# Kernel tuning notes

Hardware: AMD Instinct MI355X
Metric: run time of the kernel (lower is better)

Reference implementation:

```python
import jax, jax.numpy as jnp
import numpy as np

B, S, D_IN = 16, 1024, 1024
H, D_OUT = 16, 128

def setup_inputs() -> dict:
    key = jax.random.key(0)
    k1, k2, k3 = jax.random.split(key, 3)
    x = jax.random.normal(k1, (B, S, D_IN), dtype=jnp.float32)
    W = jax.random.normal(k2, (H, 3, D_IN, D_OUT), dtype=jnp.float32) * (1.0 / np.sqrt(D_IN))
    Wo = jax.random.normal(k3, (H * D_OUT, D_OUT), dtype=jnp.float32) * (1.0 / np.sqrt(H * D_OUT))
    return {"x": x, "W": W, "Wo": Wo}

def reference(x, W, Wo):
    # x: [B,S,D_IN], W: [H,3,D_IN,E], Wo: [H*E,E]
    E = W.shape[-1]
    q = jnp.einsum('bsd,hde->bhse', x, W[:, 0])
    k = jnp.einsum('bsd,hde->bhse', x, W[:, 1])
    v = jnp.einsum('bsd,hde->bhse', x, W[:, 2])
    # NOTE: source divides by (output_dim * 0.5), not sqrt(output_dim)
    scores = jnp.einsum('bhse,bhte->bhst', q, k) / (E * 0.5)
    attn = jax.nn.softmax(scores, axis=-1)
    o = jnp.einsum('bhst,bhte->bhse', attn, v)          # [B,H,S,E]
    o = jnp.transpose(o, (0, 2, 1, 3)).reshape(x.shape[0], x.shape[1], -1)  # concat heads
    return jnp.einsum('bsf,fe->bse', o, Wo)
```

## Files before the change

kernel.cpp:

```cpp
#include <hip/hip_runtime.h>

typedef unsigned short u16;
typedef _Float16 f16;
typedef __attribute__((ext_vector_type(8))) _Float16 half8;
typedef __attribute__((ext_vector_type(8))) short short8;
typedef __attribute__((ext_vector_type(4))) float f32x4;
typedef __attribute__((ext_vector_type(4))) float f4;
typedef __attribute__((ext_vector_type(4))) u16 u16x4;

#define B_ 16
#define S_ 1024
#define DIN_ 1024
#define H_ 16
#define E_ 128

#define EXPK 0.0225546041776533f

__device__ __forceinline__ u16 f2h(float f) {
  f16 h = (f16)f;
  return __builtin_bit_cast(u16, h);
}

__device__ __forceinline__ void gl2lds16(const u16* g, u16* l) {
  __builtin_amdgcn_global_load_lds((const __attribute__((address_space(1))) void*)g,
                                   (__attribute__((address_space(3))) void*)l, 16, 0, 0);
}

__global__ __launch_bounds__(256) void zero_f32(float* __restrict__ p) {
  int i = (blockIdx.x * 256 + threadIdx.x) * 4;
  f4 z = {0.f, 0.f, 0.f, 0.f};
  *reinterpret_cast<f4*>(p + i) = z;
}

__global__ __launch_bounds__(256) void cvt_f32_f16(const float* __restrict__ in,
                                                   u16* __restrict__ out) {
  int i = (blockIdx.x * 256 + threadIdx.x) * 4;
  f4 v = *reinterpret_cast<const f4*>(in + i);
  u16x4 o;
  o[0] = f2h(v[0]); o[1] = f2h(v[1]); o[2] = f2h(v[2]); o[3] = f2h(v[3]);
  *reinterpret_cast<u16x4*>(out + i) = o;
}

__global__ __launch_bounds__(256) void transpose_cvt(const float* __restrict__ in,
                                                     u16* __restrict__ out,
                                                     int R, int C) {
  __shared__ float tile[32][33];
  const size_t moff = (size_t)blockIdx.z * R * C;
  const float* src = in + moff;
  u16* dst = out + moff;
  int c0 = blockIdx.x * 32, r0 = blockIdx.y * 32;
  int tx = threadIdx.x & 31, ty = threadIdx.x >> 5;
#pragma unroll
  for (int i = 0; i < 32; i += 8)
    tile[ty + i][tx] = src[(size_t)(r0 + ty + i) * C + c0 + tx];
  __syncthreads();
#pragma unroll
  for (int i = 0; i < 32; i += 8)
    dst[(size_t)(c0 + ty + i) * R + r0 + tx] = f2h(tile[tx][ty + i]);
}

template<int MODE, int KSPLIT, int K>
__global__ __launch_bounds__(256) void gemm_bt(const u16* __restrict__ A,
                                               const u16* __restrict__ BT,
                                               u16* __restrict__ q, u16* __restrict__ kk,
                                               u16* __restrict__ vT, float* __restrict__ out) {
  const int tid = threadIdx.x;
  const int m0 = blockIdx.x * 128;
  const u16* Bblk = BT + (size_t)blockIdx.y * 128 * K;
  __shared__ __align__(16) u16 smem[132 * 128];
  u16* As = smem;
  u16* Bs = smem + 8192;
  const int w = tid >> 6, lane = tid & 63;
  const int quad = lane >> 4, ln = lane & 15;
  const int wr = w >> 1, wc = w & 1;

  const int kbeg = (KSPLIT > 1) ? blockIdx.z * (K / KSPLIT) : 0;
  constexpr int KLEN = K / KSPLIT;

  const int rr = lane >> 3;
  const int cc = (lane & 7) ^ rr;
  const u16* agp[4];
  const u16* bgp[4];
#pragma unroll
  for (int i = 0; i < 4; i++) {
    int row = i * 32 + w * 8 + rr;
    agp[i] = A + (size_t)(m0 + row) * K + kbeg + cc * 8;
    bgp[i] = Bblk + (size_t)row * K + kbeg + cc * 8;
  }

  int offA[4][2], offB[4][2];
#pragma unroll
  for (int mt = 0; mt < 4; mt++) {
    int row = wr * 64 + mt * 16 + ln;
#pragma unroll
    for (int k2 = 0; k2 < 2; k2++)
      offA[mt][k2] = row * 64 + (((k2 * 4 + quad) ^ (ln & 7)) * 8);
  }
#pragma unroll
  for (int nt = 0; nt < 4; nt++) {
    int row = wc * 64 + nt * 16 + ln;
#pragma unroll
    for (int k2 = 0; k2 < 2; k2++)
      offB[nt][k2] = row * 64 + (((k2 * 4 + quad) ^ (ln & 7)) * 8);
  }

  f32x4 acc[4][4];
  f32x4 zero = {0.f, 0.f, 0.f, 0.f};
#pragma unroll
  for (int mt = 0; mt < 4; mt++)
#pragma unroll
    for (int nt = 0; nt < 4; nt++) acc[mt][nt] = zero;

#pragma unroll
  for (int k0 = 0; k0 < KLEN; k0 += 64) {
    __syncthreads();
#pragma unroll
    for (int i = 0; i < 4; i++) {
      gl2lds16(agp[i] + k0, As + i * 2048 + w * 512);
      gl2lds16(bgp[i] + k0, Bs + i * 2048 + w * 512);
    }
    __syncthreads();
#pragma unroll
    for (int k2 = 0; k2 < 2; k2++) {
      half8 af[4], bfr[4];
#pragma unroll
      for (int mt = 0; mt < 4; mt++)
        af[mt] = *reinterpret_cast<const half8*>(&As[offA[mt][k2]]);
#pragma unroll
      for (int nt = 0; nt < 4; nt++)
        bfr[nt] = *reinterpret_cast<const half8*>(&Bs[offB[nt][k2]]);
#pragma unroll
      for (int mt = 0; mt < 4; mt++)
#pragma unroll
        for (int nt = 0; nt < 4; nt++)
          acc[mt][nt] = __builtin_amdgcn_mfma_f32_16x16x32_f16(af[mt], bfr[nt], acc[mt][nt], 0, 0, 0);
    }
  }

  if (MODE == 0) {
    const int h = blockIdx.y / 3, c = blockIdx.y % 3;
    if (c < 2) {
      u16* dst = (c == 0) ? q : kk;
      const float sc = (c == 0) ? EXPK : 1.0f;
#pragma unroll
      for (int mt = 0; mt < 4; mt++)
#pragma unroll
        for (int nt = 0; nt < 4; nt++)
#pragma unroll
          for (int r = 0; r < 4; r++) {
            int row = wr * 64 + mt * 16 + quad * 4 + r;
            int tok = m0 + row;
            int bb = tok >> 10, s = tok & 1023;
            int e = wc * 64 + nt * 16 + ln;
            dst[(((size_t)bb * H_ + h) * S_ + s) * E_ + e] = f2h(acc[mt][nt][r] * sc);
          }
    } else {
      __syncthreads();
#pragma unroll
      for (int mt = 0; mt < 4; mt++)
#pragma unroll
        for (int nt = 0; nt < 4; nt++)
#pragma unroll
          for (int r = 0; r < 4; r++) {
            int row = wr * 64 + mt * 16 + quad * 4 + r;
            int e = wc * 64 + nt * 16 + ln;
            smem[e * 132 + row] = f2h(acc[mt][nt][r]);
          }
      __syncthreads();
      const int bb = m0 >> 10, sbase = m0 & 1023;
      u16* vbase = vT + (((size_t)bb * H_ + h) * E_) * S_;
#pragma unroll
      for (int i = 0; i < 8; i++) {
        int e = (tid >> 4) + i * 16, s0 = (tid & 15) * 8;
        *reinterpret_cast<short8*>(&vbase[(size_t)e * S_ + sbase + s0]) =
            *reinterpret_cast<const short8*>(&smem[e * 132 + s0]);
      }
    }
  } else {
#pragma unroll
    for (int mt = 0; mt < 4; mt++)
#pragma unroll
      for (int nt = 0; nt < 4; nt++)
#pragma unroll
        for (int r = 0; r < 4; r++) {
          int row = wr * 64 + mt * 16 + quad * 4 + r;
          int e = wc * 64 + nt * 16 + ln;
          if (KSPLIT > 1)
            atomicAdd(&out[(size_t)(m0 + row) * E_ + e], acc[mt][nt][r]);
          else
            out[(size_t)(m0 + row) * E_ + e] = acc[mt][nt][r];
        }
  }
}

struct SmemKVP {
  u16 ks[64 * 128];
  u16 vs[128 * 64];
  u16 ps[128 * 68];
};
union SmemAttn {
  u16 qs[128 * 132];
  SmemKVP s;
};

__global__ __launch_bounds__(256, 3) void attn_kernel(const u16* __restrict__ qg,
                                                      const u16* __restrict__ kg,
                                                      const u16* __restrict__ vg,
                                                      u16* __restrict__ og) {
  __shared__ __align__(16) SmemAttn sm;
  const int tid = threadIdx.x;
  const int id = blockIdx.x;
  const int g = id >> 6, qt = (id >> 3) & 7, x = id & 7;
  const int hb = g * 8 + x;
  const int b = hb >> 4, h = hb & 15;
  const int q0 = qt * 128;
  const size_t bh = (size_t)(b * H_ + h);
  const u16* qp = qg + bh * S_ * E_;
  const u16* kp = kg + bh * S_ * E_;
  const u16* vp = vg + bh * E_ * S_;
  const int w = tid >> 6, lane = tid & 63, quad = lane >> 4, ln = lane & 15;

#pragma unroll
  for (int i = 0; i < 8; i++) {
    int idx = tid + i * 256;
    int row = idx >> 4, col = (idx & 15) * 8;
    *reinterpret_cast<short8*>(&sm.qs[row * 132 + col]) =
        *reinterpret_cast<const short8*>(&qp[(size_t)(q0 + row) * E_ + col]);
  }
  __syncthreads();
  half8 qf[2][4];
#pragma unroll
  for (int mt = 0; mt < 2; mt++)
#pragma unroll
    for (int ks = 0; ks < 4; ks++)
      qf[mt][ks] = *reinterpret_cast<const half8*>(
          &sm.qs[(w * 32 + mt * 16 + ln) * 132 + ks * 32 + quad * 8]);

  const int krow = w * 4 + (lane >> 4);
  const int kc = ((lane & 15) & 8) | (((lane & 15) & 7) ^ (krow & 7));
  const u16* kbase = kp + (size_t)krow * E_ + kc * 8;
  const int vrow = w * 8 + (lane >> 3);
  const int vc = (lane & 7) ^ ((lane >> 3) & 7);
  const u16* vbase = vp + (size_t)vrow * S_ + vc * 8;

  f32x4 zero = {0.f, 0.f, 0.f, 0.f};
  f32x4 oa[2][8];
#pragma unroll
  for (int mt = 0; mt < 2; mt++)
#pragma unroll
    for (int nt = 0; nt < 8; nt++) oa[mt][nt] = zero;
  float lsum[2][4];
#pragma unroll
  for (int mt = 0; mt < 2; mt++)
#pragma unroll
    for (int r = 0; r < 4; r++) lsum[mt][r] = 0.f;

  for (int kt = 0; kt < 16; kt++) {
    __syncthreads();
#pragma unroll
    for (int i = 0; i < 4; i++) {
      gl2lds16(kbase + (size_t)kt * 8192 + i * 16 * E_, &sm.s.ks[(i * 256 + w * 64) * 8]);
      gl2lds16(vbase + (size_t)kt * 64 + i * 32 * S_,   &sm.s.vs[(i * 256 + w * 64) * 8]);
    }
    __syncthreads();

    f32x4 sa[2][4];
#pragma unroll
    for (int mt = 0; mt < 2; mt++)
#pragma unroll
      for (int nt = 0; nt < 4; nt++) sa[mt][nt] = zero;
#pragma unroll
    for (int ks = 0; ks < 4; ks++) {
      half8 kf[4];
#pragma unroll
      for (int nt = 0; nt < 4; nt++) {
        int c = ks * 4 + quad;
        int cs = (c & 8) | ((c & 7) ^ (ln & 7));
        kf[nt] = *reinterpret_cast<const half8*>(&sm.s.ks[(nt * 16 + ln) * 128 + cs * 8]);
      }
#pragma unroll
      for (int mt = 0; mt < 2; mt++)
#pragma unroll
        for (int nt = 0; nt < 4; nt++)
          sa[mt][nt] = __builtin_amdgcn_mfma_f32_16x16x32_f16(qf[mt][ks], kf[nt], sa[mt][nt], 0, 0, 0);
    }

#pragma unroll
    for (int mt = 0; mt < 2; mt++) {
#pragma unroll
      for (int r = 0; r < 4; r++) {
        int prow = (w * 32 + mt * 16 + quad * 4 + r) * 68;
        float psum = 0.f;
#pragma unroll
        for (int nt = 0; nt < 4; nt++) {
          float p = exp2f(sa[mt][nt][r]);
          psum += p;
          sm.s.ps[prow + nt * 16 + ln] = f2h(p);
        }
        lsum[mt][r] += psum;
      }
    }

#pragma unroll
    for (int k2 = 0; k2 < 2; k2++) {
      half8 pf[2];
#pragma unroll
      for (int mt = 0; mt < 2; mt++)
        pf[mt] = *reinterpret_cast<const half8*>(
            &sm.s.ps[(w * 32 + mt * 16 + ln) * 68 + k2 * 32 + quad * 8]);
#pragma unroll
      for (int nt8 = 0; nt8 < 8; nt8++) {
        int c = k2 * 4 + quad;
        int cs = c ^ (ln & 7);
        half8 vf = *reinterpret_cast<const half8*>(&sm.s.vs[(nt8 * 16 + ln) * 64 + cs * 8]);
#pragma unroll
        for (int mt = 0; mt < 2; mt++)
          oa[mt][nt8] = __builtin_amdgcn_mfma_f32_16x16x32_f16(pf[mt], vf, oa[mt][nt8], 0, 0, 0);
      }
    }
  }

#pragma unroll
  for (int mt = 0; mt < 2; mt++) {
#pragma unroll
    for (int r = 0; r < 4; r++) {
      float l = lsum[mt][r];
#pragma unroll
      for (int d = 1; d < 16; d <<= 1) l += __shfl_xor(l, d);
      float rl = 1.0f / l;
      int srow = q0 + w * 32 + mt * 16 + quad * 4 + r;
      size_t base = ((size_t)b * S_ + srow) * (H_ * E_) + (size_t)h * E_;
#pragma unroll
      for (int nt8 = 0; nt8 < 8; nt8++)
        og[base + nt8 * 16 + ln] = f2h(oa[mt][nt8][r] * rl);
    }
  }
}

extern "C" void kernel_launch(void* const* d_in, const int* in_sizes, int n_in,
                              void* d_out, int out_size, void* d_ws, size_t ws_size,
                              hipStream_t stream) {
  const float* x = (const float*)d_in[0];
  const float* W = (const float*)d_in[1];
  const float* Wo = (const float*)d_in[2];
  float* out = (float*)d_out;
  char* ws = (char*)d_ws;

  const size_t WBT_BYTES = (size_t)H_ * 3 * DIN_ * E_ * 2;
  const size_t WOT_BYTES = (size_t)H_ * E_ * E_ * 2 * 2;
  const size_t FIXED = WBT_BYTES + WOT_BYTES;

  const size_t XB_PER   = (size_t)S_ * DIN_ * 2;
  const size_t QKV_PER  = (size_t)H_ * S_ * E_ * 2;
  const size_t OB_PER   = (size_t)S_ * H_ * E_ * 2;
  const size_t PER_ITEM = XB_PER + 3 * QKV_PER + OB_PER;

  int Bc = 1;
  for (int c = 16; c >= 1; c >>= 1) {
    if (FIXED + (size_t)c * PER_ITEM <= ws_size) { Bc = c; break; }
  }

  u16* WbT = (u16*)(ws);
  u16* WoT = (u16*)(ws + WBT_BYTES);
  char* cb = ws + FIXED;
  u16* xb  = (u16*)(cb);
  u16* qb  = (u16*)(cb + (size_t)Bc * XB_PER);
  u16* kb  = (u16*)(cb + (size_t)Bc * (XB_PER + QKV_PER));
  u16* vTb = (u16*)(cb + (size_t)Bc * (XB_PER + 2 * QKV_PER));
  u16* ob  = (u16*)(cb + (size_t)Bc * (XB_PER + 3 * QKV_PER));

  zero_f32<<<out_size / 1024, 256, 0, stream>>>(out);
  transpose_cvt<<<dim3(4, 32, 48), 256, 0, stream>>>(W, WbT, DIN_, E_);
  transpose_cvt<<<dim3(4, 64, 1), 256, 0, stream>>>(Wo, WoT, H_ * E_, E_);

  for (int b0 = 0; b0 < B_; b0 += Bc) {
    const float* xc = x + (size_t)b0 * S_ * DIN_;
    cvt_f32_f16<<<Bc * S_ * DIN_ / 1024, 256, 0, stream>>>(xc, xb);
    gemm_bt<0, 1, DIN_><<<dim3(Bc * 8, 48), 256, 0, stream>>>(xb, WbT, qb, kb, vTb, nullptr);
    attn_kernel<<<Bc * 128, 256, 0, stream>>>(qb, kb, vTb, ob);
    gemm_bt<1, 4, H_ * E_><<<dim3(Bc * 8, 1, 4), 256, 0, stream>>>(ob, WoT, nullptr, nullptr,
                                                                   nullptr, out + (size_t)b0 * S_ * E_);
  }
}
```

Baseline: 565.0 us.

## Keep softmax probabilities in registers by computing transposed S=K·Qᵀ

The QK^T MFMA now has its operands swapped so each lane holds score values for one query and four consecutive keys. The exp2 results are packed to fp16 in registers and used directly as the A operand of the PV MFMA, which removes the LDS round trip for P and the ps buffer. V fragments are now read as two half4 loads to match the new key ordering. Row sums are reduced across quads and redistributed with a shuffle at the end. The trade-off is more, smaller LDS reads for V in exchange for less shared memory, with possible occupancy gains.

```diff
diff --git a/kernel.cpp b/kernel.cpp
--- a/kernel.cpp
+++ b/kernel.cpp
@@ -3,6 +3,8 @@
 typedef unsigned short u16;
 typedef _Float16 f16;
 typedef __attribute__((ext_vector_type(8))) _Float16 half8;
+typedef __attribute__((ext_vector_type(4))) _Float16 half4;
+typedef __attribute__((ext_vector_type(2))) _Float16 half2v;
 typedef __attribute__((ext_vector_type(8))) short short8;
 typedef __attribute__((ext_vector_type(4))) float f32x4;
 typedef __attribute__((ext_vector_type(4))) float f4;
@@ -19,6 +21,10 @@
 __device__ __forceinline__ u16 f2h(float f) {
   f16 h = (f16)f;
   return __builtin_bit_cast(u16, h);
+}
+
+__device__ __forceinline__ half2v pkrtz(float a, float b) {
+  return __builtin_bit_cast(half2v, __builtin_amdgcn_cvt_pkrtz(a, b));
 }
 
 __device__ __forceinline__ void gl2lds16(const u16* g, u16* l) {
@@ -193,14 +199,13 @@
   }
 }
 
-struct SmemKVP {
+struct SmemKV {
   u16 ks[64 * 128];
   u16 vs[128 * 64];
-  u16 ps[128 * 68];
 };
 union SmemAttn {
   u16 qs[128 * 132];
-  SmemKVP s;
+  SmemKV s;
 };
 
 __global__ __launch_bounds__(256, 3) void attn_kernel(const u16* __restrict__ qg,
@@ -249,11 +254,9 @@
   for (int mt = 0; mt < 2; mt++)
 #pragma unroll
     for (int nt = 0; nt < 8; nt++) oa[mt][nt] = zero;
-  float lsum[2][4];
-#pragma unroll
-  for (int mt = 0; mt < 2; mt++)
-#pragma unroll
-    for (int r = 0; r < 4; r++) lsum[mt][r] = 0.f;
+  float lsum[2] = {0.f, 0.f};
+
+  const int xr = ln & 7, qh = quad >> 1, ql4 = (quad & 1) * 4;
 
   for (int kt = 0; kt < 16; kt++) {
     __syncthreads();
@@ -264,75 +267,85 @@
     }
     __syncthreads();
 
-    f32x4 sa[2][4];
-#pragma unroll
-    for (int mt = 0; mt < 2; mt++)
-#pragma unroll
-      for (int nt = 0; nt < 4; nt++) sa[mt][nt] = zero;
+    f32x4 sa[4][2];
+#pragma unroll
+    for (int t = 0; t < 4; t++)
+#pragma unroll
+      for (int nt = 0; nt < 2; nt++) sa[t][nt] = zero;
 #pragma unroll
     for (int ks = 0; ks < 4; ks++) {
       half8 kf[4];
 #pragma unroll
-      for (int nt = 0; nt < 4; nt++) {
+      for (int t = 0; t < 4; t++) {
         int c = ks * 4 + quad;
-        int cs = (c & 8) | ((c & 7) ^ (ln & 7));
-        kf[nt] = *reinterpret_cast<const half8*>(&sm.s.ks[(nt * 16 + ln) * 128 + cs * 8]);
-      }
-#pragma unroll
-      for (int mt = 0; mt < 2; mt++)
-#pragma unroll
-        for (int nt = 0; nt < 4; nt++)
-          sa[mt][nt] = __builtin_amdgcn_mfma_f32_16x16x32_f16(qf[mt][ks], kf[nt], sa[mt][nt], 0, 0, 0);
-    }
-
-#pragma unroll
-    for (int mt = 0; mt < 2; mt++) {
-#pragma unroll
-      for (int r = 0; r < 4; r++) {
-        int prow = (w * 32 + mt * 16 + quad * 4 + r) * 68;
-        float psum = 0.f;
-#pragma unroll
-        for (int nt = 0; nt < 4; nt++) {
-          float p = exp2f(sa[mt][nt][r]);
-          psum += p;
-          sm.s.ps[prow + nt * 16 + ln] = f2h(p);
-        }
-        lsum[mt][r] += psum;
-      }
-    }
-
-#pragma unroll
-    for (int k2 = 0; k2 < 2; k2++) {
+        int cs = (c & 8) | ((c & 7) ^ xr);
+        kf[t] = *reinterpret_cast<const half8*>(&sm.s.ks[(t * 16 + ln) * 128 + cs * 8]);
+      }
+#pragma unroll
+      for (int t = 0; t < 4; t++)
+#pragma unroll
+        for (int nt = 0; nt < 2; nt++)
+          sa[t][nt] = __builtin_amdgcn_mfma_f32_16x16x32_f16(kf[t], qf[nt][ks], sa[t][nt], 0, 0, 0);
+    }
+
+    half2v pk[4][2][2];
+#pragma unroll
+    for (int t = 0; t < 4; t++)
+#pragma unroll
+      for (int nt = 0; nt < 2; nt++) {
+        float p0 = exp2f(sa[t][nt][0]), p1 = exp2f(sa[t][nt][1]);
+        float p2 = exp2f(sa[t][nt][2]), p3 = exp2f(sa[t][nt][3]);
+        lsum[nt] += (p0 + p1) + (p2 + p3);
+        pk[t][nt][0] = pkrtz(p0, p1);
+        pk[t][nt][1] = pkrtz(p2, p3);
+      }
+
+#pragma unroll
+    for (int c2 = 0; c2 < 2; c2++) {
       half8 pf[2];
 #pragma unroll
-      for (int mt = 0; mt < 2; mt++)
-        pf[mt] = *reinterpret_cast<const half8*>(
-            &sm.s.ps[(w * 32 + mt * 16 + ln) * 68 + k2 * 32 + quad * 8]);
+      for (int mt = 0; mt < 2; mt++) {
+        union { half8 v8; half2v v2[4]; } u;
+        u.v2[0] = pk[2 * c2][mt][0];
+        u.v2[1] = pk[2 * c2][mt][1];
+        u.v2[2] = pk[2 * c2 + 1][mt][0];
+        u.v2[3] = pk[2 * c2 + 1][mt][1];
+        pf[mt] = u.v8;
+      }
+      const int s1 = ((4 * c2 + qh) ^ xr) * 8 + ql4;
+      const int s2 = ((4 * c2 + 2 + qh) ^ xr) * 8 + ql4;
 #pragma unroll
       for (int nt8 = 0; nt8 < 8; nt8++) {
-        int c = k2 * 4 + quad;
-        int cs = c ^ (ln & 7);
-        half8 vf = *reinterpret_cast<const half8*>(&sm.s.vs[(nt8 * 16 + ln) * 64 + cs * 8]);
+        int rowoff = (nt8 * 16 + ln) * 64;
+        union { half8 v8; half4 h4[2]; } vv;
+        vv.h4[0] = *reinterpret_cast<const half4*>(&sm.s.vs[rowoff + s1]);
+        vv.h4[1] = *reinterpret_cast<const half4*>(&sm.s.vs[rowoff + s2]);
 #pragma unroll
         for (int mt = 0; mt < 2; mt++)
-          oa[mt][nt8] = __builtin_amdgcn_mfma_f32_16x16x32_f16(pf[mt], vf, oa[mt][nt8], 0, 0, 0);
-      }
-    }
-  }
-
+          oa[mt][nt8] = __builtin_amdgcn_mfma_f32_16x16x32_f16(pf[mt], vv.v8, oa[mt][nt8], 0, 0, 0);
+      }
+    }
+  }
+
+  float rl[2];
+#pragma unroll
+  for (int nt = 0; nt < 2; nt++) {
+    float l = lsum[nt];
+    l += __shfl_xor(l, 16);
+    l += __shfl_xor(l, 32);
+    rl[nt] = 1.0f / l;
+  }
 #pragma unroll
   for (int mt = 0; mt < 2; mt++) {
 #pragma unroll
     for (int r = 0; r < 4; r++) {
-      float l = lsum[mt][r];
-#pragma unroll
-      for (int d = 1; d < 16; d <<= 1) l += __shfl_xor(l, d);
-      float rl = 1.0f / l;
+      int src = (lane & 48) | (quad * 4 + r);
+      float rlx = __shfl(rl[mt], src);
       int srow = q0 + w * 32 + mt * 16 + quad * 4 + r;
       size_t base = ((size_t)b * S_ + srow) * (H_ * E_) + (size_t)h * E_;
 #pragma unroll
       for (int nt8 = 0; nt8 < 8; nt8++)
-        og[base + nt8 * 16 + ln] = f2h(oa[mt][nt8][r] * rl);
+        og[base + nt8 * 16 + ln] = f2h(oa[mt][nt8][r] * rlx);
     }
   }
 }
```

Measured after the change: 569.2 us. Within noise of the previous version (+0.8%).
